# Kernel optimization log

Measured on AMD Instinct MI355X. Metric: run time of the kernel, lower is better.

The kernel has to match this reference:

```python
import jax, jax.numpy as jnp
import numpy as np

E = 1024   # embed_dim
H = 16     # num_heads
D = E // H # head_dim
B = 2
S = 2048
YAT_EPS = 0.1


def setup_inputs() -> dict:
    key = jax.random.key(0)
    ks = jax.random.split(key, 5)
    w_scale = (6.0 / (E + E)) ** 0.5  # xavier_uniform bound
    def xavier(k):
        return jax.random.uniform(k, (E, E), jnp.float32, -w_scale, w_scale)
    return {
        "x": jax.random.normal(ks[0], (B, S, E), jnp.float32),
        "Wq": xavier(ks[1]), "bq": jnp.zeros((E,), jnp.float32),
        "Wk": xavier(ks[2]), "bk": jnp.zeros((E,), jnp.float32),
        "Wv": xavier(ks[3]), "bv": jnp.zeros((E,), jnp.float32),
        "Wo": xavier(ks[4]), "bo": jnp.zeros((E,), jnp.float32),
    }


def reference(x, Wq, bq, Wk, bk, Wv, bv, Wo, bo):
    b, s, _ = x.shape
    # Projections (Linear: x @ W + b, flax kernel layout [in, out])
    Q = x @ Wq + bq
    K = x @ Wk + bk
    V = x @ Wv + bv
    # [B, H, S, D]
    Q = Q.reshape(b, s, H, D).transpose(0, 2, 1, 3)
    K = K.reshape(b, s, H, D).transpose(0, 2, 1, 3)
    V = V.reshape(b, s, H, D).transpose(0, 2, 1, 3)
    # L2 normalize along head_dim
    Qn = Q / (jnp.linalg.norm(Q, axis=-1, keepdims=True) + 1e-8)
    Kn = K / (jnp.linalg.norm(K, axis=-1, keepdims=True) + 1e-8)
    # Yat kernel scores: (1 + <q,k>)^2 / (eps + (1 - <q,k>))
    dot = jnp.einsum("bhqd,bhkd->bhqk", Qn, Kn)
    scores = (1.0 + dot) ** 2 / (YAT_EPS + (1.0 - dot))
    # Sum-normalize (no softmax)
    attn = scores / (jnp.sum(scores, axis=-1, keepdims=True) + 1e-6)
    out = jnp.einsum("bhqk,bhkd->bhqd", attn, V)
    out = out.transpose(0, 2, 1, 3).reshape(b, s, E)
    return out @ Wo + bo
```

## Files before the change

kernel.cpp:

```cpp
#include <hip/hip_runtime.h>
#include <math.h>

#define EDIM 1024
#define NH   16
#define HD   64
#define BATCH 2
#define SEQ  2048
#define NROW (BATCH*SEQ)
#define YAT_EPS 0.1f

typedef _Float16 f16;
typedef _Float16 f16x8 __attribute__((ext_vector_type(8)));
typedef _Float16 f16x4 __attribute__((ext_vector_type(4)));
typedef __fp16   h16x2 __attribute__((ext_vector_type(2)));
typedef float    f32x4 __attribute__((ext_vector_type(4)));

static __device__ __forceinline__ int pk2(float a, float b) {
    union { h16x2 h; int i; } u;
    u.h = __builtin_amdgcn_cvt_pkrtz(a, b);
    return u.i;
}
static __device__ __forceinline__ f16x8 cvt_f16x8(float4 a, float4 b) {
    union { int i[4]; f16x8 h; } u;
    u.i[0] = pk2(a.x, a.y);
    u.i[1] = pk2(a.z, a.w);
    u.i[2] = pk2(b.x, b.y);
    u.i[3] = pk2(b.z, b.w);
    return u.h;
}

__global__ __launch_bounds__(256)
void transcast4_kernel(const float* __restrict__ W0, const float* __restrict__ W1,
                       const float* __restrict__ W2, const float* __restrict__ W3,
                       f16* __restrict__ T0, f16* __restrict__ T1,
                       f16* __restrict__ T2, f16* __restrict__ T3)
{
    const int z = blockIdx.z;
    const float* W = (z == 0) ? W0 : (z == 1) ? W1 : (z == 2) ? W2 : W3;
    f16*         Wt = (z == 0) ? T0 : (z == 1) ? T1 : (z == 2) ? T2 : T3;

    __shared__ float T[32][33];
    const int t = threadIdx.x;
    const int r = t >> 3, c4 = (t & 7) * 4;
    const int bi = blockIdx.x * 32, bj = blockIdx.y * 32;
    const float4 v = *(const float4*)(W + (size_t)(bi + r) * 1024 + bj + c4);
    T[r][c4 + 0] = v.x; T[r][c4 + 1] = v.y; T[r][c4 + 2] = v.z; T[r][c4 + 3] = v.w;
    __syncthreads();
    f16x4 o = {(f16)T[c4 + 0][r], (f16)T[c4 + 1][r], (f16)T[c4 + 2][r], (f16)T[c4 + 3][r]};
    *(f16x4*)(Wt + (size_t)(bj + r) * 1024 + bi + c4) = o;
}

template<int BM, bool AF32>
__global__ __launch_bounds__(256)
void gemm_f16(const void* __restrict__ Av,
              const f16* __restrict__ B0, const f16* __restrict__ B1, const f16* __restrict__ B2,
              const float* __restrict__ bi0, const float* __restrict__ bi1, const float* __restrict__ bi2,
              void* __restrict__ o0, void* __restrict__ o1, void* __restrict__ o2,
              int e0, int e1, int e2)
{
    constexpr int MT   = BM / 32;
    constexpr int LA   = BM / 64;
    constexpr int ABUF = BM * 32;
    constexpr int BBUF = 128 * 32;
    constexpr int STG  = 2 * (ABUF + BBUF) * 2;
    constexpr int EPI  = BM * 128 * 2;
    constexpr int LDSB = STG > EPI ? STG : EPI;
    __shared__ __align__(16) char lds[LDSB];
    f16* As = (f16*)lds;
    f16* Bs = (f16*)lds + 2 * ABUF;

    const int z = blockIdx.z;
    const f16*   Bt   = (z == 0) ? B0  : (z == 1) ? B1  : B2;
    const float* bias = (z == 0) ? bi0 : (z == 1) ? bi1 : bi2;
    void*        Cout = (z == 0) ? o0  : (z == 1) ? o1  : o2;
    const int    epi  = (z == 0) ? e0  : (z == 1) ? e1  : e2;

    const int tid  = threadIdx.x;
    const int lane = tid & 63;
    const int w    = tid >> 6;
    const int cl   = lane & 15;
    const int quad = lane >> 4;
    const int wm = w & 1, wn = w >> 1;
    const int bm = blockIdx.x * BM, bn = blockIdx.y * 128;
    const int wmoff = wm * (MT * 16);

    const int srow = tid >> 2;
    const int sc   = tid & 3;
    const int ssw  = (sc ^ (srow & 3)) * 8;
    const float* gAf = (const float*)Av + (size_t)(bm + srow) * 1024 + sc * 8;
    const f16*   gAh = (const f16*)Av   + (size_t)(bm + srow) * 1024 + sc * 8;
    const f16*   gB  = Bt + (size_t)(bn + srow) * 1024 + sc * 8;
    int lAo[LA], lBo[2];
#pragma unroll
    for (int i = 0; i < LA; ++i) lAo[i] = (srow + i * 64) * 32 + ssw;
#pragma unroll
    for (int i = 0; i < 2;  ++i) lBo[i] = (srow + i * 64) * 32 + ssw;

    f32x4 acc[MT][4];
#pragma unroll
    for (int i = 0; i < MT; ++i)
#pragma unroll
        for (int j = 0; j < 4; ++j) acc[i][j] = (f32x4){0.f, 0.f, 0.f, 0.f};

    f16x8 ra[LA], rb[2];

#define LOAD_A(i, kn) (AF32 ? cvt_f16x8(*(const float4*)(gAf + (size_t)(i) * 64 * 1024 + (kn)),      \
                                        *(const float4*)(gAf + (size_t)(i) * 64 * 1024 + (kn) + 4))  \
                            : *(const f16x8*)(gAh + (size_t)(i) * 64 * 1024 + (kn)))

#pragma unroll
    for (int i = 0; i < LA; ++i) ra[i] = LOAD_A(i, 0);
#pragma unroll
    for (int i = 0; i < 2;  ++i) rb[i] = *(const f16x8*)(gB + (size_t)i * 64 * 1024);
#pragma unroll
    for (int i = 0; i < LA; ++i) *(f16x8*)(As + lAo[i]) = ra[i];
#pragma unroll
    for (int i = 0; i < 2;  ++i) *(f16x8*)(Bs + lBo[i]) = rb[i];
#pragma unroll
    for (int i = 0; i < LA; ++i) ra[i] = LOAD_A(i, 32);
#pragma unroll
    for (int i = 0; i < 2;  ++i) rb[i] = *(const f16x8*)(gB + (size_t)i * 64 * 1024 + 32);
    __syncthreads();

    const int fsw = (quad ^ (cl & 3)) * 8;

    for (int it = 0; it < 32; ++it) {
        const int buf = it & 1, nb = buf ^ 1;
        if (it < 31) {
#pragma unroll
            for (int i = 0; i < LA; ++i) *(f16x8*)(As + nb * ABUF + lAo[i]) = ra[i];
#pragma unroll
            for (int i = 0; i < 2;  ++i) *(f16x8*)(Bs + nb * BBUF + lBo[i]) = rb[i];
        }
        if (it < 30) {
            const int kn = (it + 2) * 32;
#pragma unroll
            for (int i = 0; i < LA; ++i) ra[i] = LOAD_A(i, kn);
#pragma unroll
            for (int i = 0; i < 2;  ++i) rb[i] = *(const f16x8*)(gB + (size_t)i * 64 * 1024 + kn);
        }
        f16x8 af[MT], bf[4];
#pragma unroll
        for (int mt = 0; mt < MT; ++mt)
            af[mt] = *(const f16x8*)(&As[buf * ABUF + (wmoff + mt * 16 + cl) * 32 + fsw]);
#pragma unroll
        for (int nt = 0; nt < 4; ++nt)
            bf[nt] = *(const f16x8*)(&Bs[buf * BBUF + (wn * 64 + nt * 16 + cl) * 32 + fsw]);
#pragma unroll
        for (int mt = 0; mt < MT; ++mt)
#pragma unroll
            for (int nt = 0; nt < 4; ++nt)
                acc[mt][nt] = __builtin_amdgcn_mfma_f32_16x16x32_f16(af[mt], bf[nt], acc[mt][nt], 0, 0, 0);
        __syncthreads();
    }
#undef LOAD_A

    float bcol[4];
#pragma unroll
    for (int nt = 0; nt < 4; ++nt) bcol[nt] = bias[bn + wn * 64 + nt * 16 + cl];
#pragma unroll
    for (int mt = 0; mt < MT; ++mt)
#pragma unroll
        for (int nt = 0; nt < 4; ++nt)
#pragma unroll
            for (int rg = 0; rg < 4; ++rg) acc[mt][nt][rg] += bcol[nt];

    const int b_idx = bm >> 11, sl0 = bm & (SEQ - 1), h0 = bn >> 6;

    if (epi == 0) {
        float* C = (float*)Cout;
#pragma unroll
        for (int mt = 0; mt < MT; ++mt)
#pragma unroll
            for (int rg = 0; rg < 4; ++rg) {
                const int row = bm + wmoff + mt * 16 + quad * 4 + rg;
#pragma unroll
                for (int nt = 0; nt < 4; ++nt)
                    C[(size_t)row * EDIM + bn + wn * 64 + nt * 16 + cl] = acc[mt][nt][rg];
            }
    } else if (epi == 1) {
        f16* C = (f16*)Cout;
        __syncthreads();
        f16* S = (f16*)lds;
#pragma unroll
        for (int mt = 0; mt < MT; ++mt)
#pragma unroll
            for (int rg = 0; rg < 4; ++rg) {
                float ss = 0.f;
#pragma unroll
                for (int nt = 0; nt < 4; ++nt) ss += acc[mt][nt][rg] * acc[mt][nt][rg];
                ss += __shfl_xor(ss, 1); ss += __shfl_xor(ss, 2);
                ss += __shfl_xor(ss, 4); ss += __shfl_xor(ss, 8);
                const float inv = 1.0f / (sqrtf(ss) + 1e-8f);
                const int row = wmoff + mt * 16 + quad * 4 + rg;
#pragma unroll
                for (int nt = 0; nt < 4; ++nt) {
                    const int col = wn * 64 + nt * 16 + cl;
                    S[row * 128 + (((col >> 3) ^ (row & 15)) * 8) + (col & 7)] =
                        (f16)(acc[mt][nt][rg] * inv);
                }
            }
        __syncthreads();
#pragma unroll
        for (int i = 0; i < BM / 16; ++i) {
            const int c = tid + i * 256;
            const int s = c >> 4, gi = c & 15;
            f16x8 v = *(const f16x8*)(&S[s * 128 + ((gi ^ (s & 15)) * 8)]);
            const int head = h0 + (gi >> 3), d8 = (gi & 7) * 8;
            *(f16x8*)(C + ((size_t)(b_idx * NH + head) * SEQ + sl0 + s) * HD + d8) = v;
        }
    } else {
        f16* C = (f16*)Cout;
        __syncthreads();
        f16* S = (f16*)lds;
        constexpr int GM = BM / 8 - 1;
#pragma unroll
        for (int mt = 0; mt < MT; ++mt) {
            const int s0 = wmoff + mt * 16 + quad * 4;
#pragma unroll
            for (int nt = 0; nt < 4; ++nt) {
                const int col = wn * 64 + nt * 16 + cl;
                f16x4 o = {(f16)acc[mt][nt][0], (f16)acc[mt][nt][1],
                           (f16)acc[mt][nt][2], (f16)acc[mt][nt][3]};
                *(f16x4*)(&S[col * BM + (((s0 >> 3) ^ (col & GM)) * 8) + (s0 & 7)]) = o;
            }
        }
        __syncthreads();
        constexpr int GSH = (BM == 128) ? 4 : 3;
#pragma unroll
        for (int i = 0; i < BM / 16; ++i) {
            const int c = tid + i * 256;
            const int col = c >> GSH, gi = c & GM;
            f16x8 v = *(const f16x8*)(&S[col * BM + ((gi ^ (col & GM)) * 8)]);
            const int head = h0 + (col >> 6), d = col & 63;
            *(f16x8*)(C + ((size_t)(b_idx * NH + head) * HD + d) * SEQ + sl0 + gi * 8) = v;
        }
    }
}

__global__ __launch_bounds__(512, 4)
void yat_attn(const f16* __restrict__ Qh, const f16* __restrict__ Kh,
              const f16* __restrict__ Vt, f16* __restrict__ AO)
{
    __shared__ __align__(16) char lds[49152];
    f16* Qs = (f16*)lds;
    f16* KB = (f16*)(lds + 16384);
    f16* VB = (f16*)(lds + 32768);

    const int tid  = threadIdx.x;
    const int lane = tid & 63;
    const int w    = tid >> 6;
    const int cl   = lane & 15;
    const int quad = lane >> 4;
    const int wm = w & 3;
    const int wk = w >> 2;
    const int q0 = blockIdx.x * 128;
    const int bh = blockIdx.y;

    const f16* Qg = Qh + (size_t)bh * SEQ * HD;
    const f16* Kg = Kh + (size_t)bh * SEQ * HD;
    const f16* Vg = Vt + (size_t)bh * HD * SEQ;

    const int rkv = tid >> 3;
    const int gkv = tid & 7;
    const f16* gK = Kg + (size_t)rkv * HD + gkv * 8;
    const f16* gV = Vg + (size_t)rkv * SEQ + gkv * 8;
    const int lkOff = rkv * 64 + ((gkv ^ (rkv & 7)) * 8);

    f16x8 kr = *(const f16x8*)(gK);
    f16x8 vr = *(const f16x8*)(gV);

#pragma unroll
    for (int i = 0; i < 2; ++i) {
        const int s0 = tid + i * 512;
        const int row = s0 >> 3, g = s0 & 7;
        f16x8 v = *(const f16x8*)(Qg + (size_t)(q0 + row) * HD + g * 8);
        *(f16x8*)(&Qs[row * 64 + ((g ^ (row & 7)) * 8)]) = v;
    }
    __syncthreads();
    f16x8 qf[2][2];
#pragma unroll
    for (int qt = 0; qt < 2; ++qt)
#pragma unroll
        for (int kb = 0; kb < 2; ++kb)
            qf[qt][kb] = *(const f16x8*)(&Qs[(wm * 32 + qt * 16 + cl) * 64 +
                                             ((kb * 4 + quad) ^ (cl & 7)) * 8]);

    f32x4 O[2][4];
    float rs[2] = {0.f, 0.f};
#pragma unroll
    for (int i = 0; i < 2; ++i)
#pragma unroll
        for (int j = 0; j < 4; ++j) O[i][j] = (f32x4){0.f, 0.f, 0.f, 0.f};

    const int addrA = ((((quad & 1) << 1) * 16) + cl) << 2;
    const int addrB = addrA + 64;

    for (int t = 0; t < 32; ++t) {
        const int buf = t & 1;
        *(f16x8*)(&KB[buf * 4096 + lkOff]) = kr;
        *(f16x8*)(&VB[buf * 4096 + lkOff]) = vr;
        if (t < 31) {
            kr = *(const f16x8*)(gK + (size_t)(t + 1) * 64 * HD);
            vr = *(const f16x8*)(gV + (t + 1) * 64);
        }
        __syncthreads();

        const f16* Ks = KB + buf * 4096;
        const f16* Vs = VB + buf * 4096;

        f32x4 s[2][2];
#pragma unroll
        for (int kt = 0; kt < 2; ++kt)
#pragma unroll
            for (int qt = 0; qt < 2; ++qt) s[kt][qt] = (f32x4){0.f, 0.f, 0.f, 0.f};
#pragma unroll
        for (int kb = 0; kb < 2; ++kb) {
            const int sw = ((kb * 4 + quad) ^ (cl & 7)) * 8;
            f16x8 af0 = *(const f16x8*)(&Ks[(wk * 32 +  0 + cl) * 64 + sw]);
            f16x8 af1 = *(const f16x8*)(&Ks[(wk * 32 + 16 + cl) * 64 + sw]);
#pragma unroll
            for (int qt = 0; qt < 2; ++qt) {
                s[0][qt] = __builtin_amdgcn_mfma_f32_16x16x32_f16(af0, qf[qt][kb], s[0][qt], 0, 0, 0);
                s[1][qt] = __builtin_amdgcn_mfma_f32_16x16x32_f16(af1, qf[qt][kb], s[1][qt], 0, 0, 0);
            }
        }

        int pks[2][2][2];
#pragma unroll
        for (int kt = 0; kt < 2; ++kt)
#pragma unroll
            for (int qt = 0; qt < 2; ++qt) {
                float p[4];
#pragma unroll
                for (int rg = 0; rg < 4; ++rg) {
                    const float u = (1.0f + YAT_EPS) - s[kt][qt][rg];
                    p[rg] = fmaf(4.41f, __builtin_amdgcn_rcpf(u), u - 4.2f);
                    rs[qt] += p[rg];
                }
                pks[kt][qt][0] = pk2(p[0], p[1]);
                pks[kt][qt][1] = pk2(p[2], p[3]);
            }

        f16x8 pa[2];
#pragma unroll
        for (int qt = 0; qt < 2; ++qt) {
            union { int i[4]; f16x8 h; } u;
#pragma unroll
            for (int j = 0; j < 2; ++j) {
                int a0 = __builtin_amdgcn_ds_bpermute(addrA, pks[0][qt][j]);
                int a1 = __builtin_amdgcn_ds_bpermute(addrA, pks[1][qt][j]);
                u.i[j]     = (quad >= 2) ? a1 : a0;
                int b0 = __builtin_amdgcn_ds_bpermute(addrB, pks[0][qt][j]);
                int b1 = __builtin_amdgcn_ds_bpermute(addrB, pks[1][qt][j]);
                u.i[j + 2] = (quad >= 2) ? b1 : b0;
            }
            pa[qt] = u.h;
        }

#pragma unroll
        for (int dn = 0; dn < 4; ++dn) {
            f16x8 vb = *(const f16x8*)(&Vs[(dn * 16 + cl) * 64 +
                                           ((wk * 4 + quad) ^ (cl & 7)) * 8]);
#pragma unroll
            for (int qt = 0; qt < 2; ++qt)
                O[qt][dn] = __builtin_amdgcn_mfma_f32_16x16x32_f16(pa[qt], vb, O[qt][dn], 0, 0, 0);
        }
    }

    __syncthreads();
    float* rs_s = (float*)lds;
    float* Ox   = (float*)(lds + 1024);

#pragma unroll
    for (int qt = 0; qt < 2; ++qt) {
        float t = rs[qt];
        t += __shfl_xor(t, 16);
        t += __shfl_xor(t, 32);
        if (quad == 0) rs_s[wk * 128 + wm * 32 + qt * 16 + cl] = t;
    }
    if (wk == 1) {
#pragma unroll
        for (int qt = 0; qt < 2; ++qt)
#pragma unroll
            for (int dn = 0; dn < 4; ++dn)
#pragma unroll
                for (int rg = 0; rg < 4; ++rg)
                    Ox[(wm * 32 + qt * 16 + quad * 4 + rg) * 64 + dn * 16 + cl] = O[qt][dn][rg];
    }
    __syncthreads();
    if (wk == 0) {
        const int b = bh >> 4, h = bh & 15;
#pragma unroll
        for (int qt = 0; qt < 2; ++qt)
#pragma unroll
            for (int rg = 0; rg < 4; ++rg) {
                const int ql = wm * 32 + qt * 16 + quad * 4 + rg;
                const float tot = rs_s[ql] + rs_s[128 + ql];
                const float inv = 1.0f / (tot + 1e-6f);
                const size_t rowoff = ((size_t)b * SEQ + q0 + ql) * EDIM + h * 64;
#pragma unroll
                for (int dn = 0; dn < 4; ++dn)
                    AO[rowoff + dn * 16 + cl] =
                        (f16)((O[qt][dn][rg] + Ox[ql * 64 + dn * 16 + cl]) * inv);
            }
    }
}

extern "C" void kernel_launch(void* const* d_in, const int* in_sizes, int n_in,
                              void* d_out, int out_size, void* d_ws, size_t ws_size,
                              hipStream_t stream)
{
    const float* x  = (const float*)d_in[0];
    const float* Wq = (const float*)d_in[1];
    const float* bq = (const float*)d_in[2];
    const float* Wk = (const float*)d_in[3];
    const float* bk = (const float*)d_in[4];
    const float* Wv = (const float*)d_in[5];
    const float* bv = (const float*)d_in[6];
    const float* Wo = (const float*)d_in[7];
    const float* bo = (const float*)d_in[8];

    char* p = (char*)d_ws;
    f16* Wqt = (f16*)p;                 p += (size_t)EDIM * EDIM * 2;
    f16* Wkt = (f16*)p;                 p += (size_t)EDIM * EDIM * 2;
    f16* Wvt = (f16*)p;                 p += (size_t)EDIM * EDIM * 2;
    f16* Wot = (f16*)p;                 p += (size_t)EDIM * EDIM * 2;
    f16* Qhb = (f16*)p;                 p += (size_t)NROW * EDIM * 2;
    f16* Khb = (f16*)p;                 p += (size_t)NROW * EDIM * 2;
    f16* Vtb = (f16*)p;                 p += (size_t)NROW * EDIM * 2;
    f16* AOb = (f16*)p;                 p += (size_t)NROW * EDIM * 2;

    transcast4_kernel<<<dim3(32, 32, 4), 256, 0, stream>>>(Wq, Wk, Wv, Wo,
                                                           Wqt, Wkt, Wvt, Wot);

    gemm_f16<128, true><<<dim3(NROW / 128, EDIM / 128, 3), 256, 0, stream>>>(
        x, Wqt, Wkt, Wvt, bq, bk, bv, Qhb, Khb, Vtb, 1, 1, 2);

    yat_attn<<<dim3(SEQ / 128, BATCH * NH), 512, 0, stream>>>(Qhb, Khb, Vtb, AOb);

    gemm_f16<64, false><<<dim3(NROW / 64, EDIM / 128, 1), 256, 0, stream>>>(
        AOb, Wot, Wot, Wot, bo, bo, bo, d_out, d_out, d_out, 0, 0, 0);
}
```

Baseline: 205.6 us.

## Load K/V fragments directly from global and drop shared-memory staging barriers

Removes the block-wide LDS double buffer for K and V and the per-iteration __syncthreads. Each wave now loads its own MFMA fragments straight from global memory, with K prefetched one tile ahead and V loaded in the same iteration. The P transpose moves from ds_bpermute shuffles to a small per-wave LDS scratch buffer, and Q fragments are read directly from global. The aim is to cut barrier and LDS traffic, at the cost of redundant global/L2 reads across waves sharing tiles and more exposed load latency.

```diff
diff --git a/kernel.cpp b/kernel.cpp
--- a/kernel.cpp
+++ b/kernel.cpp
@@ -242,10 +242,7 @@
 void yat_attn(const f16* __restrict__ Qh, const f16* __restrict__ Kh,
               const f16* __restrict__ Vt, f16* __restrict__ AO)
 {
-    __shared__ __align__(16) char lds[49152];
-    f16* Qs = (f16*)lds;
-    f16* KB = (f16*)(lds + 16384);
-    f16* VB = (f16*)(lds + 32768);
+    __shared__ __align__(16) char lds[33792];
 
     const int tid  = threadIdx.x;
     const int lane = tid & 63;
@@ -261,30 +258,18 @@
     const f16* Kg = Kh + (size_t)bh * SEQ * HD;
     const f16* Vg = Vt + (size_t)bh * HD * SEQ;
 
-    const int rkv = tid >> 3;
-    const int gkv = tid & 7;
-    const f16* gK = Kg + (size_t)rkv * HD + gkv * 8;
-    const f16* gV = Vg + (size_t)rkv * SEQ + gkv * 8;
-    const int lkOff = rkv * 64 + ((gkv ^ (rkv & 7)) * 8);
-
-    f16x8 kr = *(const f16x8*)(gK);
-    f16x8 vr = *(const f16x8*)(gV);
-
-#pragma unroll
-    for (int i = 0; i < 2; ++i) {
-        const int s0 = tid + i * 512;
-        const int row = s0 >> 3, g = s0 & 7;
-        f16x8 v = *(const f16x8*)(Qg + (size_t)(q0 + row) * HD + g * 8);
-        *(f16x8*)(&Qs[row * 64 + ((g ^ (row & 7)) * 8)]) = v;
-    }
-    __syncthreads();
     f16x8 qf[2][2];
 #pragma unroll
     for (int qt = 0; qt < 2; ++qt)
 #pragma unroll
         for (int kb = 0; kb < 2; ++kb)
-            qf[qt][kb] = *(const f16x8*)(&Qs[(wm * 32 + qt * 16 + cl) * 64 +
-                                             ((kb * 4 + quad) ^ (cl & 7)) * 8]);
+            qf[qt][kb] = *(const f16x8*)(Qg + (size_t)(q0 + wm * 32 + qt * 16 + cl) * HD +
+                                         (kb * 4 + quad) * 8);
+
+    const f16* gKf = Kg + (size_t)(wk * 32 + cl) * HD + quad * 8;
+    const f16* gVf = Vg + (size_t)cl * SEQ + wk * 32 + quad * 8;
+
+    f16* Pw = (f16*)lds + w * 1152;
 
     f32x4 O[2][4];
     float rs[2] = {0.f, 0.f};
@@ -293,21 +278,27 @@
 #pragma unroll
         for (int j = 0; j < 4; ++j) O[i][j] = (f32x4){0.f, 0.f, 0.f, 0.f};
 
-    const int addrA = ((((quad & 1) << 1) * 16) + cl) << 2;
-    const int addrB = addrA + 64;
-
+    f16x8 kc[4];
+#pragma unroll
+    for (int kt = 0; kt < 2; ++kt)
+#pragma unroll
+        for (int kb = 0; kb < 2; ++kb)
+            kc[kt * 2 + kb] = *(const f16x8*)(gKf + (size_t)(kt * 16) * HD + kb * 32);
+
+#pragma unroll 2
     for (int t = 0; t < 32; ++t) {
-        const int buf = t & 1;
-        *(f16x8*)(&KB[buf * 4096 + lkOff]) = kr;
-        *(f16x8*)(&VB[buf * 4096 + lkOff]) = vr;
+        f16x8 vc[4];
+#pragma unroll
+        for (int dn = 0; dn < 4; ++dn)
+            vc[dn] = *(const f16x8*)(gVf + (size_t)(dn * 16) * SEQ + t * 64);
+        f16x8 kn[4];
         if (t < 31) {
-            kr = *(const f16x8*)(gK + (size_t)(t + 1) * 64 * HD);
-            vr = *(const f16x8*)(gV + (t + 1) * 64);
-        }
-        __syncthreads();
-
-        const f16* Ks = KB + buf * 4096;
-        const f16* Vs = VB + buf * 4096;
+#pragma unroll
+            for (int kt = 0; kt < 2; ++kt)
+#pragma unroll
+                for (int kb = 0; kb < 2; ++kb)
+                    kn[kt * 2 + kb] = *(const f16x8*)(gKf + (size_t)((t + 1) * 64 + kt * 16) * HD + kb * 32);
+        }
 
         f32x4 s[2][2];
 #pragma unroll
@@ -315,18 +306,13 @@
 #pragma unroll
             for (int qt = 0; qt < 2; ++qt) s[kt][qt] = (f32x4){0.f, 0.f, 0.f, 0.f};
 #pragma unroll
-        for (int kb = 0; kb < 2; ++kb) {
-            const int sw = ((kb * 4 + quad) ^ (cl & 7)) * 8;
-            f16x8 af0 = *(const f16x8*)(&Ks[(wk * 32 +  0 + cl) * 64 + sw]);
-            f16x8 af1 = *(const f16x8*)(&Ks[(wk * 32 + 16 + cl) * 64 + sw]);
+        for (int kb = 0; kb < 2; ++kb)
 #pragma unroll
             for (int qt = 0; qt < 2; ++qt) {
-                s[0][qt] = __builtin_amdgcn_mfma_f32_16x16x32_f16(af0, qf[qt][kb], s[0][qt], 0, 0, 0);
-                s[1][qt] = __builtin_amdgcn_mfma_f32_16x16x32_f16(af1, qf[qt][kb], s[1][qt], 0, 0, 0);
-            }
-        }
-
-        int pks[2][2][2];
+                s[0][qt] = __builtin_amdgcn_mfma_f32_16x16x32_f16(kc[0 * 2 + kb], qf[qt][kb], s[0][qt], 0, 0, 0);
+                s[1][qt] = __builtin_amdgcn_mfma_f32_16x16x32_f16(kc[1 * 2 + kb], qf[qt][kb], s[1][qt], 0, 0, 0);
+            }
+
 #pragma unroll
         for (int kt = 0; kt < 2; ++kt)
 #pragma unroll
@@ -338,34 +324,25 @@
                     p[rg] = fmaf(4.41f, __builtin_amdgcn_rcpf(u), u - 4.2f);
                     rs[qt] += p[rg];
                 }
-                pks[kt][qt][0] = pk2(p[0], p[1]);
-                pks[kt][qt][1] = pk2(p[2], p[3]);
+                union { int i[2]; f16x4 h; } pk;
+                pk.i[0] = pk2(p[0], p[1]);
+                pk.i[1] = pk2(p[2], p[3]);
+                *(f16x4*)(&Pw[(qt * 16 + cl) * 36 + kt * 16 + quad * 4]) = pk.h;
             }
 
         f16x8 pa[2];
 #pragma unroll
-        for (int qt = 0; qt < 2; ++qt) {
-            union { int i[4]; f16x8 h; } u;
-#pragma unroll
-            for (int j = 0; j < 2; ++j) {
-                int a0 = __builtin_amdgcn_ds_bpermute(addrA, pks[0][qt][j]);
-                int a1 = __builtin_amdgcn_ds_bpermute(addrA, pks[1][qt][j]);
-                u.i[j]     = (quad >= 2) ? a1 : a0;
-                int b0 = __builtin_amdgcn_ds_bpermute(addrB, pks[0][qt][j]);
-                int b1 = __builtin_amdgcn_ds_bpermute(addrB, pks[1][qt][j]);
-                u.i[j + 2] = (quad >= 2) ? b1 : b0;
-            }
-            pa[qt] = u.h;
-        }
-
-#pragma unroll
-        for (int dn = 0; dn < 4; ++dn) {
-            f16x8 vb = *(const f16x8*)(&Vs[(dn * 16 + cl) * 64 +
-                                           ((wk * 4 + quad) ^ (cl & 7)) * 8]);
+        for (int qt = 0; qt < 2; ++qt)
+            pa[qt] = *(const f16x8*)(&Pw[(qt * 16 + cl) * 36 + quad * 8]);
+
+#pragma unroll
+        for (int dn = 0; dn < 4; ++dn)
 #pragma unroll
             for (int qt = 0; qt < 2; ++qt)
-                O[qt][dn] = __builtin_amdgcn_mfma_f32_16x16x32_f16(pa[qt], vb, O[qt][dn], 0, 0, 0);
-        }
+                O[qt][dn] = __builtin_amdgcn_mfma_f32_16x16x32_f16(pa[qt], vc[dn], O[qt][dn], 0, 0, 0);
+
+#pragma unroll
+        for (int i = 0; i < 4; ++i) kc[i] = kn[i];
     }
 
     __syncthreads();
```

New measurement: 269.7 us. 31.2% more time.

## Precast x to f16 and retile projection GEMMs to larger blocks

Applied to the files above, without the earlier changes.

Adds a separate kernel that converts x to f16 once, so the QKV GEMM loads f16 directly instead of converting fp32 in its inner loop. The GEMM is reworked to a fixed 128-row tile with a templated N width: the QKV projection uses 128x256 tiles with 512 threads, and the output projection moves from 64x128 to 128x128 tiles. The epilogues stage two heads at a time through shared memory to fit the smaller buffer. The goal is more reuse per tile and a lighter main loop, at the cost of an extra launch and an extra pass over x in memory, plus fewer blocks for the output GEMM.

```diff
diff --git a/kernel.cpp b/kernel.cpp
--- a/kernel.cpp
+++ b/kernel.cpp
@@ -20,13 +20,16 @@
     u.h = __builtin_amdgcn_cvt_pkrtz(a, b);
     return u.i;
 }
-static __device__ __forceinline__ f16x8 cvt_f16x8(float4 a, float4 b) {
-    union { int i[4]; f16x8 h; } u;
-    u.i[0] = pk2(a.x, a.y);
-    u.i[1] = pk2(a.z, a.w);
-    u.i[2] = pk2(b.x, b.y);
-    u.i[3] = pk2(b.z, b.w);
-    return u.h;
+
+__global__ __launch_bounds__(256)
+void cast_f16_kernel(const float* __restrict__ src, f16* __restrict__ dst)
+{
+    const int i = (blockIdx.x * 256 + threadIdx.x) * 4;
+    const float4 v = *(const float4*)(src + i);
+    union { int i[2]; f16x4 h; } o;
+    o.i[0] = pk2(v.x, v.y);
+    o.i[1] = pk2(v.z, v.w);
+    *(f16x4*)(dst + i) = o.h;
 }
 
 __global__ __launch_bounds__(256)
@@ -50,22 +53,21 @@
     *(f16x4*)(Wt + (size_t)(bj + r) * 1024 + bi + c4) = o;
 }
 
-template<int BM, bool AF32>
-__global__ __launch_bounds__(256)
-void gemm_f16(const void* __restrict__ Av,
+template<int BN>
+__global__ __launch_bounds__(BN * 2, 2)
+void gemm_f16(const f16* __restrict__ A,
               const f16* __restrict__ B0, const f16* __restrict__ B1, const f16* __restrict__ B2,
               const float* __restrict__ bi0, const float* __restrict__ bi1, const float* __restrict__ bi2,
               void* __restrict__ o0, void* __restrict__ o1, void* __restrict__ o2,
               int e0, int e1, int e2)
 {
-    constexpr int MT   = BM / 32;
-    constexpr int LA   = BM / 64;
-    constexpr int ABUF = BM * 32;
-    constexpr int BBUF = 128 * 32;
-    constexpr int STG  = 2 * (ABUF + BBUF) * 2;
-    constexpr int EPI  = BM * 128 * 2;
-    constexpr int LDSB = STG > EPI ? STG : EPI;
-    __shared__ __align__(16) char lds[LDSB];
+    constexpr int NT   = BN * 2;
+    constexpr int SR   = NT / 4;
+    constexpr int ASL  = 128 / SR;
+    constexpr int BSL  = BN / SR;
+    constexpr int ABUF = 128 * 32;
+    constexpr int BBUF = BN * 32;
+    __shared__ __align__(16) char lds[2 * (ABUF + BBUF) * 2];
     f16* As = (f16*)lds;
     f16* Bs = (f16*)lds + 2 * ABUF;
 
@@ -81,45 +83,40 @@
     const int cl   = lane & 15;
     const int quad = lane >> 4;
     const int wm = w & 1, wn = w >> 1;
-    const int bm = blockIdx.x * BM, bn = blockIdx.y * 128;
-    const int wmoff = wm * (MT * 16);
+    const int bm = blockIdx.x * 128, bn = blockIdx.y * BN;
+    const int wmoff = wm * 64;
 
     const int srow = tid >> 2;
     const int sc   = tid & 3;
     const int ssw  = (sc ^ (srow & 3)) * 8;
-    const float* gAf = (const float*)Av + (size_t)(bm + srow) * 1024 + sc * 8;
-    const f16*   gAh = (const f16*)Av   + (size_t)(bm + srow) * 1024 + sc * 8;
-    const f16*   gB  = Bt + (size_t)(bn + srow) * 1024 + sc * 8;
-    int lAo[LA], lBo[2];
-#pragma unroll
-    for (int i = 0; i < LA; ++i) lAo[i] = (srow + i * 64) * 32 + ssw;
-#pragma unroll
-    for (int i = 0; i < 2;  ++i) lBo[i] = (srow + i * 64) * 32 + ssw;
-
-    f32x4 acc[MT][4];
-#pragma unroll
-    for (int i = 0; i < MT; ++i)
+    const f16* gA = A  + (size_t)(bm + srow) * 1024 + sc * 8;
+    const f16* gB = Bt + (size_t)(bn + srow) * 1024 + sc * 8;
+    int lAo[ASL], lBo[BSL];
+#pragma unroll
+    for (int i = 0; i < ASL; ++i) lAo[i] = (srow + i * SR) * 32 + ssw;
+#pragma unroll
+    for (int i = 0; i < BSL; ++i) lBo[i] = (srow + i * SR) * 32 + ssw;
+
+    f32x4 acc[4][4];
+#pragma unroll
+    for (int i = 0; i < 4; ++i)
 #pragma unroll
         for (int j = 0; j < 4; ++j) acc[i][j] = (f32x4){0.f, 0.f, 0.f, 0.f};
 
-    f16x8 ra[LA], rb[2];
-
-#define LOAD_A(i, kn) (AF32 ? cvt_f16x8(*(const float4*)(gAf + (size_t)(i) * 64 * 1024 + (kn)),      \
-                                        *(const float4*)(gAf + (size_t)(i) * 64 * 1024 + (kn) + 4))  \
-                            : *(const f16x8*)(gAh + (size_t)(i) * 64 * 1024 + (kn)))
-
-#pragma unroll
-    for (int i = 0; i < LA; ++i) ra[i] = LOAD_A(i, 0);
-#pragma unroll
-    for (int i = 0; i < 2;  ++i) rb[i] = *(const f16x8*)(gB + (size_t)i * 64 * 1024);
-#pragma unroll
-    for (int i = 0; i < LA; ++i) *(f16x8*)(As + lAo[i]) = ra[i];
-#pragma unroll
-    for (int i = 0; i < 2;  ++i) *(f16x8*)(Bs + lBo[i]) = rb[i];
-#pragma unroll
-    for (int i = 0; i < LA; ++i) ra[i] = LOAD_A(i, 32);
-#pragma unroll
-    for (int i = 0; i < 2;  ++i) rb[i] = *(const f16x8*)(gB + (size_t)i * 64 * 1024 + 32);
+    f16x8 ra[ASL], rb[BSL];
+
+#pragma unroll
+    for (int i = 0; i < ASL; ++i) ra[i] = *(const f16x8*)(gA + (size_t)i * SR * 1024);
+#pragma unroll
+    for (int i = 0; i < BSL; ++i) rb[i] = *(const f16x8*)(gB + (size_t)i * SR * 1024);
+#pragma unroll
+    for (int i = 0; i < ASL; ++i) *(f16x8*)(As + lAo[i]) = ra[i];
+#pragma unroll
+    for (int i = 0; i < BSL; ++i) *(f16x8*)(Bs + lBo[i]) = rb[i];
+#pragma unroll
+    for (int i = 0; i < ASL; ++i) ra[i] = *(const f16x8*)(gA + (size_t)i * SR * 1024 + 32);
+#pragma unroll
+    for (int i = 0; i < BSL; ++i) rb[i] = *(const f16x8*)(gB + (size_t)i * SR * 1024 + 32);
     __syncthreads();
 
     const int fsw = (quad ^ (cl & 3)) * 8;
@@ -128,38 +125,37 @@
         const int buf = it & 1, nb = buf ^ 1;
         if (it < 31) {
 #pragma unroll
-            for (int i = 0; i < LA; ++i) *(f16x8*)(As + nb * ABUF + lAo[i]) = ra[i];
-#pragma unroll
-            for (int i = 0; i < 2;  ++i) *(f16x8*)(Bs + nb * BBUF + lBo[i]) = rb[i];
+            for (int i = 0; i < ASL; ++i) *(f16x8*)(As + nb * ABUF + lAo[i]) = ra[i];
+#pragma unroll
+            for (int i = 0; i < BSL; ++i) *(f16x8*)(Bs + nb * BBUF + lBo[i]) = rb[i];
         }
         if (it < 30) {
             const int kn = (it + 2) * 32;
 #pragma unroll
-            for (int i = 0; i < LA; ++i) ra[i] = LOAD_A(i, kn);
-#pragma unroll
-            for (int i = 0; i < 2;  ++i) rb[i] = *(const f16x8*)(gB + (size_t)i * 64 * 1024 + kn);
-        }
-        f16x8 af[MT], bf[4];
-#pragma unroll
-        for (int mt = 0; mt < MT; ++mt)
+            for (int i = 0; i < ASL; ++i) ra[i] = *(const f16x8*)(gA + (size_t)i * SR * 1024 + kn);
+#pragma unroll
+            for (int i = 0; i < BSL; ++i) rb[i] = *(const f16x8*)(gB + (size_t)i * SR * 1024 + kn);
+        }
+        f16x8 af[4], bf[4];
+#pragma unroll
+        for (int mt = 0; mt < 4; ++mt)
             af[mt] = *(const f16x8*)(&As[buf * ABUF + (wmoff + mt * 16 + cl) * 32 + fsw]);
 #pragma unroll
         for (int nt = 0; nt < 4; ++nt)
             bf[nt] = *(const f16x8*)(&Bs[buf * BBUF + (wn * 64 + nt * 16 + cl) * 32 + fsw]);
 #pragma unroll
-        for (int mt = 0; mt < MT; ++mt)
+        for (int mt = 0; mt < 4; ++mt)
 #pragma unroll
             for (int nt = 0; nt < 4; ++nt)
                 acc[mt][nt] = __builtin_amdgcn_mfma_f32_16x16x32_f16(af[mt], bf[nt], acc[mt][nt], 0, 0, 0);
         __syncthreads();
     }
-#undef LOAD_A
 
     float bcol[4];
 #pragma unroll
     for (int nt = 0; nt < 4; ++nt) bcol[nt] = bias[bn + wn * 64 + nt * 16 + cl];
 #pragma unroll
-    for (int mt = 0; mt < MT; ++mt)
+    for (int mt = 0; mt < 4; ++mt)
 #pragma unroll
         for (int nt = 0; nt < 4; ++nt)
 #pragma unroll
@@ -170,7 +166,7 @@
     if (epi == 0) {
         float* C = (float*)Cout;
 #pragma unroll
-        for (int mt = 0; mt < MT; ++mt)
+        for (int mt = 0; mt < 4; ++mt)
 #pragma unroll
             for (int rg = 0; rg < 4; ++rg) {
                 const int row = bm + wmoff + mt * 16 + quad * 4 + rg;
@@ -180,60 +176,68 @@
             }
     } else if (epi == 1) {
         f16* C = (f16*)Cout;
-        __syncthreads();
         f16* S = (f16*)lds;
 #pragma unroll
-        for (int mt = 0; mt < MT; ++mt)
-#pragma unroll
-            for (int rg = 0; rg < 4; ++rg) {
-                float ss = 0.f;
-#pragma unroll
-                for (int nt = 0; nt < 4; ++nt) ss += acc[mt][nt][rg] * acc[mt][nt][rg];
-                ss += __shfl_xor(ss, 1); ss += __shfl_xor(ss, 2);
-                ss += __shfl_xor(ss, 4); ss += __shfl_xor(ss, 8);
-                const float inv = 1.0f / (sqrtf(ss) + 1e-8f);
-                const int row = wmoff + mt * 16 + quad * 4 + rg;
-#pragma unroll
-                for (int nt = 0; nt < 4; ++nt) {
-                    const int col = wn * 64 + nt * 16 + cl;
-                    S[row * 128 + (((col >> 3) ^ (row & 15)) * 8) + (col & 7)] =
-                        (f16)(acc[mt][nt][rg] * inv);
-                }
-            }
-        __syncthreads();
-#pragma unroll
-        for (int i = 0; i < BM / 16; ++i) {
-            const int c = tid + i * 256;
-            const int s = c >> 4, gi = c & 15;
-            f16x8 v = *(const f16x8*)(&S[s * 128 + ((gi ^ (s & 15)) * 8)]);
-            const int head = h0 + (gi >> 3), d8 = (gi & 7) * 8;
-            *(f16x8*)(C + ((size_t)(b_idx * NH + head) * SEQ + sl0 + s) * HD + d8) = v;
+        for (int h = 0; h < 2; ++h) {
+            __syncthreads();
+            if ((wn >> 1) == h) {
+#pragma unroll
+                for (int mt = 0; mt < 4; ++mt)
+#pragma unroll
+                    for (int rg = 0; rg < 4; ++rg) {
+                        float ss = 0.f;
+#pragma unroll
+                        for (int nt = 0; nt < 4; ++nt) ss += acc[mt][nt][rg] * acc[mt][nt][rg];
+                        ss += __shfl_xor(ss, 1); ss += __shfl_xor(ss, 2);
+                        ss += __shfl_xor(ss, 4); ss += __shfl_xor(ss, 8);
+                        const float inv = 1.0f / (sqrtf(ss) + 1e-8f);
+                        const int row = wmoff + mt * 16 + quad * 4 + rg;
+#pragma unroll
+                        for (int nt = 0; nt < 4; ++nt) {
+                            const int colh = (wn & 1) * 64 + nt * 16 + cl;
+                            S[row * 128 + (((colh >> 3) ^ (row & 15)) * 8) + (colh & 7)] =
+                                (f16)(acc[mt][nt][rg] * inv);
+                        }
+                    }
+            }
+            __syncthreads();
+#pragma unroll
+            for (int i = 0; i < 4; ++i) {
+                const int c = tid + i * NT;
+                const int s = c >> 4, gi = c & 15;
+                f16x8 v = *(const f16x8*)(&S[s * 128 + ((gi ^ (s & 15)) * 8)]);
+                const int head = h0 + h * 2 + (gi >> 3), d8 = (gi & 7) * 8;
+                *(f16x8*)(C + ((size_t)(b_idx * NH + head) * SEQ + sl0 + s) * HD + d8) = v;
+            }
         }
     } else {
         f16* C = (f16*)Cout;
-        __syncthreads();
         f16* S = (f16*)lds;
-        constexpr int GM = BM / 8 - 1;
-#pragma unroll
-        for (int mt = 0; mt < MT; ++mt) {
-            const int s0 = wmoff + mt * 16 + quad * 4;
-#pragma unroll
-            for (int nt = 0; nt < 4; ++nt) {
-                const int col = wn * 64 + nt * 16 + cl;
-                f16x4 o = {(f16)acc[mt][nt][0], (f16)acc[mt][nt][1],
-                           (f16)acc[mt][nt][2], (f16)acc[mt][nt][3]};
-                *(f16x4*)(&S[col * BM + (((s0 >> 3) ^ (col & GM)) * 8) + (s0 & 7)]) = o;
-            }
-        }
-        __syncthreads();
-        constexpr int GSH = (BM == 128) ? 4 : 3;
-#pragma unroll
-        for (int i = 0; i < BM / 16; ++i) {
-            const int c = tid + i * 256;
-            const int col = c >> GSH, gi = c & GM;
-            f16x8 v = *(const f16x8*)(&S[col * BM + ((gi ^ (col & GM)) * 8)]);
-            const int head = h0 + (col >> 6), d = col & 63;
-            *(f16x8*)(C + ((size_t)(b_idx * NH + head) * HD + d) * SEQ + sl0 + gi * 8) = v;
+#pragma unroll
+        for (int h = 0; h < 2; ++h) {
+            __syncthreads();
+            if ((wn >> 1) == h) {
+#pragma unroll
+                for (int mt = 0; mt < 4; ++mt) {
+                    const int s0 = wmoff + mt * 16 + quad * 4;
+#pragma unroll
+                    for (int nt = 0; nt < 4; ++nt) {
+                        const int colh = (wn & 1) * 64 + nt * 16 + cl;
+                        f16x4 o = {(f16)acc[mt][nt][0], (f16)acc[mt][nt][1],
+                                   (f16)acc[mt][nt][2], (f16)acc[mt][nt][3]};
+                        *(f16x4*)(&S[colh * 128 + (((s0 >> 3) ^ (colh & 15)) * 8) + (s0 & 7)]) = o;
+                    }
+                }
+            }
+            __syncthreads();
+#pragma unroll
+            for (int i = 0; i < 4; ++i) {
+                const int c = tid + i * NT;
+                const int colh = c >> 4, gi = c & 15;
+                f16x8 v = *(const f16x8*)(&S[colh * 128 + ((gi ^ (colh & 15)) * 8)]);
+                const int head = h0 + h * 2 + (colh >> 6), d = colh & 63;
+                *(f16x8*)(C + ((size_t)(b_idx * NH + head) * HD + d) * SEQ + sl0 + gi * 8) = v;
+            }
         }
     }
 }
@@ -422,6 +426,7 @@
     const float* bo = (const float*)d_in[8];
 
     char* p = (char*)d_ws;
+    f16* xb  = (f16*)p;                 p += (size_t)NROW * EDIM * 2;
     f16* Wqt = (f16*)p;                 p += (size_t)EDIM * EDIM * 2;
     f16* Wkt = (f16*)p;                 p += (size_t)EDIM * EDIM * 2;
     f16* Wvt = (f16*)p;                 p += (size_t)EDIM * EDIM * 2;
@@ -431,14 +436,15 @@
     f16* Vtb = (f16*)p;                 p += (size_t)NROW * EDIM * 2;
     f16* AOb = (f16*)p;                 p += (size_t)NROW * EDIM * 2;
 
+    cast_f16_kernel<<<NROW * EDIM / 1024, 256, 0, stream>>>(x, xb);
     transcast4_kernel<<<dim3(32, 32, 4), 256, 0, stream>>>(Wq, Wk, Wv, Wo,
                                                            Wqt, Wkt, Wvt, Wot);
 
-    gemm_f16<128, true><<<dim3(NROW / 128, EDIM / 128, 3), 256, 0, stream>>>(
-        x, Wqt, Wkt, Wvt, bq, bk, bv, Qhb, Khb, Vtb, 1, 1, 2);
+    gemm_f16<256><<<dim3(NROW / 128, EDIM / 256, 3), 512, 0, stream>>>(
+        xb, Wqt, Wkt, Wvt, bq, bk, bv, Qhb, Khb, Vtb, 1, 1, 2);
 
     yat_attn<<<dim3(SEQ / 128, BATCH * NH), 512, 0, stream>>>(Qhb, Khb, Vtb, AOb);
 
-    gemm_f16<64, false><<<dim3(NROW / 64, EDIM / 128, 1), 256, 0, stream>>>(
+    gemm_f16<128><<<dim3(NROW / 128, EDIM / 128, 1), 256, 0, stream>>>(
         AOb, Wot, Wot, Wot, bo, bo, bo, d_out, d_out, d_out, 0, 0, 0);
 }
```

Result: no change. 204.4 us (-0.6%).
